# Performance work log

Measured on AMD Instinct MI355X. Metric: run time of the kernel, lower is better.

The kernel has to match this reference:

```python
import jax, jax.numpy as jnp
import numpy as np

M = 41
RHO = M / 2.0          # rho=-1 -> M/2
OVERLAPS = 40

def _get_index():
    S = [(n1, n2)
         for n1 in range(-(M // 2), M // 2)
         for n2 in range(-(M // 2), M // 2)
         if abs(n1 * n2) <= RHO * (M // 2)]
    return np.asarray(S, dtype=np.int32)  # [K,2], K=1600 for defaults

_PAIRS = _get_index()


def setup_inputs() -> dict:
    key = jax.random.key(0)
    ks = jax.random.split(key, 7)
    B, L, N = 2, 2048, 2
    K = _PAIRS.shape[0]
    return {
        "x_real": jax.random.normal(ks[0], (B, L, N), jnp.float32),
        "x_imag": jax.random.normal(ks[1], (B, L, N), jnp.float32),
        "task_info": jax.random.uniform(ks[2], (B, 4), jnp.float32),
        "fc_wr": jax.random.normal(ks[3], (K,), jnp.float32) * 0.02,
        "fc_wi": jax.random.normal(ks[4], (K,), jnp.float32) * 0.02,
        "fc_br": jax.random.normal(ks[5], (1,), jnp.float32) * 0.02,
        "fc_bi": jax.random.normal(ks[6], (1,), jnp.float32) * 0.02,
    }


def reference(x_real, x_imag, task_info, fc_wr, fc_wi, fc_br, fc_bi):
    B, L, N = x_real.shape
    x0 = x_real + 1j * x_imag                      # [B,L,N] complex64
    # get_power: dBm -> Watts per mode
    P = 1e-3 * jnp.power(10.0, task_info[:, 0] / 10.0) / N   # [B]

    xf = jnp.fft.fft(x0, axis=1)                   # [B,L,N]
    idx = jnp.arange(L)
    n1 = jnp.asarray(_PAIRS[:, 0])
    n2 = jnp.asarray(_PAIRS[:, 1])

    # torch.roll(x, s, dim=1)[i] == x[(i - s) % L]; vectorize over all K pairs
    def gather(s):                                  # s: [K]
        return xf[:, (idx[:, None] - s[None, :]) % L, :]   # [B,L,K,N]

    A = gather(n1) * jnp.conj(gather(n1 + n2))      # [B,L,K,N]
    E = (A + jnp.roll(A, 1, axis=-1)) * gather(n2)  # [B,L,K,N]

    w = fc_wr + 1j * fc_wi                          # [K]
    b = fc_br[0] + 1j * fc_bi[0]
    delta = jnp.einsum('blkn,k->bln', E, w) + b     # ComplexLinear K->1
    delta = jnp.fft.ifft(delta, axis=1)

    out = (x0 + delta * P[:, None, None])[:, OVERLAPS // 2 : L - OVERLAPS // 2, :]
    # return real/imag stacked so the baseline output is real-valued
    return jnp.stack([out.real, out.imag], axis=-1)  # [B, L-OVERLAPS, N, 2]
```

## Files before the change

kernel.cpp:

```cpp
#include <hip/hip_runtime.h>


#define L_FFT 2048
#define NB 2
#define NM 2
#define ND 40
#define CROP 20
#define LOUT 2008

__device__ __forceinline__ float2 cmul(float2 a, float2 b) {
    return make_float2(a.x*b.x - a.y*b.y, a.x*b.y + a.y*b.x);
}
__device__ __forceinline__ float2 cmulc(float2 a, float2 b) {
    return make_float2(a.x*b.x + a.y*b.y, a.y*b.x - a.x*b.y);
}

template<int SIGN, int NT>
__device__ void build_tw(float2* tw, int tid) {
    for (int t = tid; t < 1024; t += NT) {
        float ang = (float)(SIGN * t) * 3.0679615757712823e-03f;
        tw[t] = make_float2(__cosf(ang), __sinf(ang));
    }
}

template<int NT>
__device__ float2* fft2048(float2* bufA, float2* bufB, const float2* tw, int tid) {
    float2* src = bufA;
    float2* dst = bufB;
    int m = 1;
    for (int stage = 0; stage < 11; ++stage) {
        __syncthreads();
        #pragma unroll
        for (int it = 0; it < 1024 / NT; ++it) {
            int q = tid + it * NT;
            int k = q & (m - 1);
            int jm = q - k;
            float2 w = tw[jm];
            float2 a = src[q];
            float2 b = src[q + 1024];
            float2 dif = make_float2(a.x - b.x, a.y - b.y);
            dst[2*jm + k]     = make_float2(a.x + b.x, a.y + b.y);
            dst[2*jm + k + m] = make_float2(dif.x*w.x - dif.y*w.y, dif.x*w.y + dif.y*w.x);
        }
        float2* t = src; src = dst; dst = t;
        m <<= 1;
    }
    __syncthreads();
    return src;
}

__global__ __launch_bounds__(1024) void fft_fwd_kernel(const float* __restrict__ xr,
                                                       const float* __restrict__ xi,
                                                       float2* __restrict__ xf,
                                                       float* __restrict__ df) {
    __shared__ float2 bufA[L_FFT];
    __shared__ float2 bufB[L_FFT];
    __shared__ float2 tw[1024];
    int bn = blockIdx.x;
    int b = bn >> 1, n = bn & 1;
    int tid = threadIdx.x;
    #pragma unroll
    for (int i = 0; i < 4; ++i)
        df[bn * (L_FFT * 2) + tid + i * 1024] = 0.f;
    for (int t = tid; t < L_FFT; t += 1024) {
        int gi = (b * L_FFT + t) * NM + n;
        bufA[t] = make_float2(xr[gi], xi[gi]);
    }
    build_tw<-1, 1024>(tw, tid);
    float2* res = fft2048<1024>(bufA, bufB, tw, tid);
    for (int f = tid; f < L_FFT; f += 1024)
        xf[bn * L_FFT + f] = res[f];
}

__global__ __launch_bounds__(256) void gs2_kernel(const float2* __restrict__ xf,
                                                  const float* __restrict__ wr,
                                                  const float* __restrict__ wi,
                                                  float* __restrict__ df) {
    __shared__ float2 xs[2][336];
    __shared__ float2 Gs[296];
    __shared__ float wrs[40], wis[40];
    int blk = blockIdx.x;
    int b   = blk / 320;
    int rem = blk % 320;
    int d   = rem >> 3;
    int l0  = (rem & 7) << 8;
    int dd  = d - 20;
    int tid = threadIdx.x;
    const float2* x0 = xf + (b * 2 + 0) * L_FFT;
    const float2* x1 = xf + (b * 2 + 1) * L_FFT;
    for (int i = tid; i < 336; i += 256) {
        int m = (l0 - 39 + i) & (L_FFT - 1);
        xs[0][i] = x0[m];
        xs[1][i] = x1[m];
    }
    if (tid < 40) { wrs[tid] = wr[tid * 40 + d]; wis[tid] = wi[tid * 40 + d]; }
    __syncthreads();
    for (int j = tid; j < 295; j += 256) {
        float2 g0 = cmulc(xs[0][j + 20], xs[0][j + 20 - dd]);
        float2 g1 = cmulc(xs[1][j + 20], xs[1][j + 20 - dd]);
        Gs[j] = make_float2(g0.x + g1.x, g0.y + g1.y);
    }
    __syncthreads();
    float2 acc = make_float2(0.f, 0.f);
    #pragma unroll
    for (int n1i = 0; n1i < 40; ++n1i) {
        float2 g = Gs[tid + 39 - n1i];
        float wxr = wrs[n1i], wxi = wis[n1i];
        acc.x += wxr * g.x - wxi * g.y;
        acc.y += wxr * g.y + wxi * g.x;
    }
    int xvi = tid + 39 - dd;
    int base = (b * 2) * (L_FFT * 2) + (l0 + tid) * 2;
    float2 xv0 = xs[0][xvi];
    float2 c0 = cmul(acc, xv0);
    unsafeAtomicAdd(&df[base + 0], c0.x);
    unsafeAtomicAdd(&df[base + 1], c0.y);
    float2 xv1 = xs[1][xvi];
    float2 c1 = cmul(acc, xv1);
    unsafeAtomicAdd(&df[base + L_FFT * 2 + 0], c1.x);
    unsafeAtomicAdd(&df[base + L_FFT * 2 + 1], c1.y);
}

__global__ __launch_bounds__(1024) void ifft_out_kernel(const float* __restrict__ df,
                                                        const float* __restrict__ xr,
                                                        const float* __restrict__ xi,
                                                        const float* __restrict__ task,
                                                        float* __restrict__ out) {
    __shared__ float2 bufA[L_FFT];
    __shared__ float2 bufB[L_FFT];
    __shared__ float2 tw[1024];
    int bn = blockIdx.x;
    int b = bn >> 1, n = bn & 1;
    int tid = threadIdx.x;
    const float2* dfreq = (const float2*)df + bn * L_FFT;
    for (int i = tid; i < L_FFT; i += 1024)
        bufA[i] = dfreq[i];
    build_tw<1, 1024>(tw, tid);
    float2* res = fft2048<1024>(bufA, bufB, tw, tid);
    float P = 1e-3f * __powf(10.f, task[b * 4] * 0.1f) * 0.5f;
    float scale = P * (1.0f / (float)L_FFT);
    for (int t = CROP + tid; t < L_FFT - CROP; t += 1024) {
        int gi = (b * L_FFT + t) * NM + n;
        float2 dv = res[t];
        int oi = ((b * LOUT + (t - CROP)) * NM + n) * 2;
        out[oi]     = xr[gi] + dv.x * scale;
        out[oi + 1] = xi[gi] + dv.y * scale;
    }
}

extern "C" void kernel_launch(void* const* d_in, const int* in_sizes, int n_in,
                              void* d_out, int out_size, void* d_ws, size_t ws_size,
                              hipStream_t stream) {
    const float* xr   = (const float*)d_in[0];
    const float* xi   = (const float*)d_in[1];
    const float* task = (const float*)d_in[2];
    const float* wr   = (const float*)d_in[3];
    const float* wi   = (const float*)d_in[4];
    float* out = (float*)d_out;

    float2* ws = (float2*)d_ws;
    float2* xf = ws;
    float*  df = (float*)(ws + 8192);

    hipLaunchKernelGGL(fft_fwd_kernel, dim3(NB * NM), dim3(1024), 0, stream, xr, xi, xf, df);
    hipLaunchKernelGGL(gs2_kernel,     dim3(NB * ND * 8), dim3(256), 0, stream, xf, wr, wi, df);
    hipLaunchKernelGGL(ifft_out_kernel, dim3(NB * NM), dim3(1024), 0, stream, df, xr, xi, task, out);
}
```

Baseline: 22.73 us.

## Fuse FFT, gather-sum and IFFT into one cooperative kernel with grid syncs

```diff
diff --git a/kernel.cpp b/kernel.cpp
--- a/kernel.cpp
+++ b/kernel.cpp
@@ -1,4 +1,7 @@
 #include <hip/hip_runtime.h>
+#include <hip/hip_cooperative_groups.h>
+
+namespace cg = cooperative_groups;
 
 
 #define L_FFT 2048
@@ -7,6 +10,11 @@
 #define ND 40
 #define CROP 20
 #define LOUT 2008
+#define NBLK 160
+#define NT 1024
+#define TILE 1024
+#define SLAB 1103
+#define GSZ 1063
 
 __device__ __forceinline__ float2 cmul(float2 a, float2 b) {
     return make_float2(a.x*b.x - a.y*b.y, a.x*b.y + a.y*b.x);
@@ -15,7 +23,7 @@
     return make_float2(a.x*b.x + a.y*b.y, a.y*b.x - a.x*b.y);
 }
 
-template<int SIGN, int NT>
+template<int SIGN>
 __device__ void build_tw(float2* tw, int tid) {
     for (int t = tid; t < 1024; t += NT) {
         float ang = (float)(SIGN * t) * 3.0679615757712823e-03f;
@@ -23,16 +31,14 @@
     }
 }
 
-template<int NT>
 __device__ float2* fft2048(float2* bufA, float2* bufB, const float2* tw, int tid) {
     float2* src = bufA;
     float2* dst = bufB;
     int m = 1;
     for (int stage = 0; stage < 11; ++stage) {
         __syncthreads();
-        #pragma unroll
-        for (int it = 0; it < 1024 / NT; ++it) {
-            int q = tid + it * NT;
+        {
+            int q = tid;
             int k = q & (m - 1);
             int jm = q - k;
             float2 w = tw[jm];
@@ -49,102 +55,102 @@
     return src;
 }
 
-__global__ __launch_bounds__(1024) void fft_fwd_kernel(const float* __restrict__ xr,
-                                                       const float* __restrict__ xi,
-                                                       float2* __restrict__ xf,
-                                                       float* __restrict__ df) {
-    __shared__ float2 bufA[L_FFT];
-    __shared__ float2 bufB[L_FFT];
-    __shared__ float2 tw[1024];
-    int bn = blockIdx.x;
-    int b = bn >> 1, n = bn & 1;
+__global__ __launch_bounds__(NT) void fused_kernel(const float* __restrict__ xr,
+                                                   const float* __restrict__ xi,
+                                                   const float* __restrict__ task,
+                                                   const float* __restrict__ wr,
+                                                   const float* __restrict__ wi,
+                                                   float* __restrict__ out,
+                                                   float2* __restrict__ xf,
+                                                   float* __restrict__ df) {
+    cg::grid_group grid = cg::this_grid();
+    __shared__ float2 sm[5120];
+    __shared__ float wrs[ND], wis[ND];
+    int blk = blockIdx.x;
     int tid = threadIdx.x;
-    #pragma unroll
-    for (int i = 0; i < 4; ++i)
-        df[bn * (L_FFT * 2) + tid + i * 1024] = 0.f;
-    for (int t = tid; t < L_FFT; t += 1024) {
-        int gi = (b * L_FFT + t) * NM + n;
-        bufA[t] = make_float2(xr[gi], xi[gi]);
+
+    if (blk < NB * NM) {
+        int b = blk >> 1, n = blk & 1;
+        float2* bufA = sm;
+        float2* bufB = sm + 2048;
+        float2* tw   = sm + 4096;
+        float2* dfv = (float2*)df + blk * L_FFT;
+        #pragma unroll
+        for (int i = 0; i < 2; ++i)
+            dfv[tid + i * NT] = make_float2(0.f, 0.f);
+        for (int t = tid; t < L_FFT; t += NT) {
+            int gi = (b * L_FFT + t) * NM + n;
+            bufA[t] = make_float2(xr[gi], xi[gi]);
+        }
+        build_tw<-1>(tw, tid);
+        float2* res = fft2048(bufA, bufB, tw, tid);
+        for (int f = tid; f < L_FFT; f += NT)
+            xf[blk * L_FFT + f] = res[f];
     }
-    build_tw<-1, 1024>(tw, tid);
-    float2* res = fft2048<1024>(bufA, bufB, tw, tid);
-    for (int f = tid; f < L_FFT; f += 1024)
-        xf[bn * L_FFT + f] = res[f];
-}
+    grid.sync();
 
-__global__ __launch_bounds__(256) void gs2_kernel(const float2* __restrict__ xf,
-                                                  const float* __restrict__ wr,
-                                                  const float* __restrict__ wi,
-                                                  float* __restrict__ df) {
-    __shared__ float2 xs[2][336];
-    __shared__ float2 Gs[296];
-    __shared__ float wrs[40], wis[40];
-    int blk = blockIdx.x;
-    int b   = blk / 320;
-    int rem = blk % 320;
-    int d   = rem >> 3;
-    int l0  = (rem & 7) << 8;
-    int dd  = d - 20;
-    int tid = threadIdx.x;
-    const float2* x0 = xf + (b * 2 + 0) * L_FFT;
-    const float2* x1 = xf + (b * 2 + 1) * L_FFT;
-    for (int i = tid; i < 336; i += 256) {
-        int m = (l0 - 39 + i) & (L_FFT - 1);
-        xs[0][i] = x0[m];
-        xs[1][i] = x1[m];
+    {
+        int b   = blk / 80;
+        int rem = blk % 80;
+        int d   = rem >> 1;
+        int l0  = (rem & 1) << 10;
+        int dd  = d - 20;
+        float2* xs0 = sm;
+        float2* xs1 = sm + SLAB;
+        float2* Gs  = sm + 2 * SLAB;
+        const float2* x0 = xf + (b * 2 + 0) * L_FFT;
+        const float2* x1 = xf + (b * 2 + 1) * L_FFT;
+        for (int i = tid; i < SLAB; i += NT) {
+            int m = (l0 - 39 + i) & (L_FFT - 1);
+            xs0[i] = x0[m];
+            xs1[i] = x1[m];
+        }
+        if (tid < ND) { wrs[tid] = wr[tid * ND + d]; wis[tid] = wi[tid * ND + d]; }
+        __syncthreads();
+        for (int j = tid; j < GSZ; j += NT) {
+            float2 g0 = cmulc(xs0[j + 20], xs0[j + 20 - dd]);
+            float2 g1 = cmulc(xs1[j + 20], xs1[j + 20 - dd]);
+            Gs[j] = make_float2(g0.x + g1.x, g0.y + g1.y);
+        }
+        __syncthreads();
+        float2 acc = make_float2(0.f, 0.f);
+        #pragma unroll
+        for (int n1i = 0; n1i < ND; ++n1i) {
+            float2 g = Gs[tid + 39 - n1i];
+            float wxr = wrs[n1i], wxi = wis[n1i];
+            acc.x += wxr * g.x - wxi * g.y;
+            acc.y += wxr * g.y + wxi * g.x;
+        }
+        int xvi  = tid + 39 - dd;
+        int base = (b * 2) * (L_FFT * 2) + (l0 + tid) * 2;
+        float2 c0 = cmul(acc, xs0[xvi]);
+        unsafeAtomicAdd(&df[base + 0], c0.x);
+        unsafeAtomicAdd(&df[base + 1], c0.y);
+        float2 c1 = cmul(acc, xs1[xvi]);
+        unsafeAtomicAdd(&df[base + L_FFT * 2 + 0], c1.x);
+        unsafeAtomicAdd(&df[base + L_FFT * 2 + 1], c1.y);
     }
-    if (tid < 40) { wrs[tid] = wr[tid * 40 + d]; wis[tid] = wi[tid * 40 + d]; }
-    __syncthreads();
-    for (int j = tid; j < 295; j += 256) {
-        float2 g0 = cmulc(xs[0][j + 20], xs[0][j + 20 - dd]);
-        float2 g1 = cmulc(xs[1][j + 20], xs[1][j + 20 - dd]);
-        Gs[j] = make_float2(g0.x + g1.x, g0.y + g1.y);
-    }
-    __syncthreads();
-    float2 acc = make_float2(0.f, 0.f);
-    #pragma unroll
-    for (int n1i = 0; n1i < 40; ++n1i) {
-        float2 g = Gs[tid + 39 - n1i];
-        float wxr = wrs[n1i], wxi = wis[n1i];
-        acc.x += wxr * g.x - wxi * g.y;
-        acc.y += wxr * g.y + wxi * g.x;
-    }
-    int xvi = tid + 39 - dd;
-    int base = (b * 2) * (L_FFT * 2) + (l0 + tid) * 2;
-    float2 xv0 = xs[0][xvi];
-    float2 c0 = cmul(acc, xv0);
-    unsafeAtomicAdd(&df[base + 0], c0.x);
-    unsafeAtomicAdd(&df[base + 1], c0.y);
-    float2 xv1 = xs[1][xvi];
-    float2 c1 = cmul(acc, xv1);
-    unsafeAtomicAdd(&df[base + L_FFT * 2 + 0], c1.x);
-    unsafeAtomicAdd(&df[base + L_FFT * 2 + 1], c1.y);
-}
+    grid.sync();
 
-__global__ __launch_bounds__(1024) void ifft_out_kernel(const float* __restrict__ df,
-                                                        const float* __restrict__ xr,
-                                                        const float* __restrict__ xi,
-                                                        const float* __restrict__ task,
-                                                        float* __restrict__ out) {
-    __shared__ float2 bufA[L_FFT];
-    __shared__ float2 bufB[L_FFT];
-    __shared__ float2 tw[1024];
-    int bn = blockIdx.x;
-    int b = bn >> 1, n = bn & 1;
-    int tid = threadIdx.x;
-    const float2* dfreq = (const float2*)df + bn * L_FFT;
-    for (int i = tid; i < L_FFT; i += 1024)
-        bufA[i] = dfreq[i];
-    build_tw<1, 1024>(tw, tid);
-    float2* res = fft2048<1024>(bufA, bufB, tw, tid);
-    float P = 1e-3f * __powf(10.f, task[b * 4] * 0.1f) * 0.5f;
-    float scale = P * (1.0f / (float)L_FFT);
-    for (int t = CROP + tid; t < L_FFT - CROP; t += 1024) {
-        int gi = (b * L_FFT + t) * NM + n;
-        float2 dv = res[t];
-        int oi = ((b * LOUT + (t - CROP)) * NM + n) * 2;
-        out[oi]     = xr[gi] + dv.x * scale;
-        out[oi + 1] = xi[gi] + dv.y * scale;
+    if (blk < NB * NM) {
+        int b = blk >> 1, n = blk & 1;
+        float2* bufA = sm;
+        float2* bufB = sm + 2048;
+        float2* tw   = sm + 4096;
+        const float2* dfreq = (const float2*)df + blk * L_FFT;
+        for (int i = tid; i < L_FFT; i += NT)
+            bufA[i] = dfreq[i];
+        build_tw<1>(tw, tid);
+        float2* res = fft2048(bufA, bufB, tw, tid);
+        float P = 1e-3f * __powf(10.f, task[b * 4] * 0.1f) * 0.5f;
+        float scale = P * (1.0f / (float)L_FFT);
+        for (int t = CROP + tid; t < L_FFT - CROP; t += NT) {
+            int gi = (b * L_FFT + t) * NM + n;
+            float2 dv = res[t];
+            int oi = ((b * LOUT + (t - CROP)) * NM + n) * 2;
+            out[oi]     = xr[gi] + dv.x * scale;
+            out[oi + 1] = xi[gi] + dv.y * scale;
+        }
     }
 }
 
@@ -162,7 +168,7 @@
     float2* xf = ws;
     float*  df = (float*)(ws + 8192);
 
-    hipLaunchKernelGGL(fft_fwd_kernel, dim3(NB * NM), dim3(1024), 0, stream, xr, xi, xf, df);
-    hipLaunchKernelGGL(gs2_kernel,     dim3(NB * ND * 8), dim3(256), 0, stream, xf, wr, wi, df);
-    hipLaunchKernelGGL(ifft_out_kernel, dim3(NB * NM), dim3(1024), 0, stream, df, xr, xi, task, out);
+    void* args[] = { (void*)&xr, (void*)&xi, (void*)&task, (void*)&wr, (void*)&wi,
+                     (void*)&out, (void*)&xf, (void*)&df };
+    hipLaunchCooperativeKernel((void*)fused_kernel, dim3(NBLK), dim3(NT), args, 0, stream);
 }
```

Measured after the change: 61.82 us. +171.9%, slower.

## Switch FFTs to radix-4 Stockham and merge four shift offsets per gs2 block

Applied to the files above, without the earlier changes.

```diff
diff --git a/kernel.cpp b/kernel.cpp
--- a/kernel.cpp
+++ b/kernel.cpp
@@ -15,131 +15,165 @@
     return make_float2(a.x*b.x + a.y*b.y, a.y*b.x - a.x*b.y);
 }
 
-template<int SIGN, int NT>
+template<int SIGN>
 __device__ void build_tw(float2* tw, int tid) {
-    for (int t = tid; t < 1024; t += NT) {
-        float ang = (float)(SIGN * t) * 3.0679615757712823e-03f;
-        tw[t] = make_float2(__cosf(ang), __sinf(ang));
-    }
-}
-
-template<int NT>
-__device__ float2* fft2048(float2* bufA, float2* bufB, const float2* tw, int tid) {
+    if (tid < 512) {
+        float ang = (float)(SIGN * tid) * 3.0679615757712823e-03f;
+        tw[tid] = make_float2(__cosf(ang), __sinf(ang));
+    }
+}
+
+template<int SIGN>
+__device__ float2* fft2048_r4(float2* bufA, float2* bufB, const float2* tw, int tid) {
     float2* src = bufA;
     float2* dst = bufB;
-    int m = 1;
-    for (int stage = 0; stage < 11; ++stage) {
+    #pragma unroll
+    for (int m = 1; m <= 256; m *= 4) {
         __syncthreads();
-        #pragma unroll
-        for (int it = 0; it < 1024 / NT; ++it) {
-            int q = tid + it * NT;
-            int k = q & (m - 1);
-            int jm = q - k;
-            float2 w = tw[jm];
-            float2 a = src[q];
-            float2 b = src[q + 1024];
-            float2 dif = make_float2(a.x - b.x, a.y - b.y);
-            dst[2*jm + k]     = make_float2(a.x + b.x, a.y + b.y);
-            dst[2*jm + k + m] = make_float2(dif.x*w.x - dif.y*w.y, dif.x*w.y + dif.y*w.x);
-        }
+        int k2 = tid & (m - 1);
+        int jm = tid - k2;
+        float2 A = src[tid];
+        float2 C = src[tid + 512];
+        float2 B = src[tid + 1024];
+        float2 D = src[tid + 1536];
+        float2 T0 = make_float2(A.x + B.x, A.y + B.y);
+        float2 T1 = make_float2(A.x - B.x, A.y - B.y);
+        float2 T2 = make_float2(C.x + D.x, C.y + D.y);
+        float2 cd = make_float2(C.x - D.x, C.y - D.y);
+        float2 T3 = (SIGN < 0) ? make_float2(cd.y, -cd.x)
+                               : make_float2(-cd.y, cd.x);
+        float2 w1 = tw[jm];
+        float2 w2 = cmul(w1, w1);
+        float2 w3 = cmul(w2, w1);
+        int base = 4 * jm + k2;
+        dst[base]         = make_float2(T0.x + T2.x, T0.y + T2.y);
+        dst[base + m]     = cmul(make_float2(T1.x + T3.x, T1.y + T3.y), w1);
+        dst[base + 2*m]   = cmul(make_float2(T0.x - T2.x, T0.y - T2.y), w2);
+        dst[base + 3*m]   = cmul(make_float2(T1.x - T3.x, T1.y - T3.y), w3);
         float2* t = src; src = dst; dst = t;
-        m <<= 1;
     }
     __syncthreads();
-    return src;
-}
-
-__global__ __launch_bounds__(1024) void fft_fwd_kernel(const float* __restrict__ xr,
-                                                       const float* __restrict__ xi,
-                                                       float2* __restrict__ xf,
-                                                       float* __restrict__ df) {
+    #pragma unroll
+    for (int it = 0; it < 2; ++it) {
+        int q = tid + it * 512;
+        float2 a = src[q];
+        float2 b = src[q + 1024];
+        dst[q]        = make_float2(a.x + b.x, a.y + b.y);
+        dst[q + 1024] = make_float2(a.x - b.x, a.y - b.y);
+    }
+    float2* res = dst;
+    __syncthreads();
+    return res;
+}
+
+__global__ __launch_bounds__(512) void fft_fwd_kernel(const float* __restrict__ xr,
+                                                      const float* __restrict__ xi,
+                                                      float2* __restrict__ xf,
+                                                      float* __restrict__ df) {
     __shared__ float2 bufA[L_FFT];
     __shared__ float2 bufB[L_FFT];
-    __shared__ float2 tw[1024];
+    __shared__ float2 tw[512];
     int bn = blockIdx.x;
     int b = bn >> 1, n = bn & 1;
     int tid = threadIdx.x;
     #pragma unroll
-    for (int i = 0; i < 4; ++i)
-        df[bn * (L_FFT * 2) + tid + i * 1024] = 0.f;
-    for (int t = tid; t < L_FFT; t += 1024) {
+    for (int i = 0; i < 8; ++i)
+        df[bn * (L_FFT * 2) + tid + i * 512] = 0.f;
+    #pragma unroll
+    for (int it = 0; it < 4; ++it) {
+        int t = tid + it * 512;
         int gi = (b * L_FFT + t) * NM + n;
         bufA[t] = make_float2(xr[gi], xi[gi]);
     }
-    build_tw<-1, 1024>(tw, tid);
-    float2* res = fft2048<1024>(bufA, bufB, tw, tid);
-    for (int f = tid; f < L_FFT; f += 1024)
+    build_tw<-1>(tw, tid);
+    float2* res = fft2048_r4<-1>(bufA, bufB, tw, tid);
+    #pragma unroll
+    for (int it = 0; it < 4; ++it) {
+        int f = tid + it * 512;
         xf[bn * L_FFT + f] = res[f];
+    }
 }
 
 __global__ __launch_bounds__(256) void gs2_kernel(const float2* __restrict__ xf,
                                                   const float* __restrict__ wr,
                                                   const float* __restrict__ wi,
                                                   float* __restrict__ df) {
-    __shared__ float2 xs[2][336];
+    __shared__ float2 xs0[336], xs1[336];
     __shared__ float2 Gs[296];
-    __shared__ float wrs[40], wis[40];
+    __shared__ float wrs[40][4], wis[40][4];
     int blk = blockIdx.x;
-    int b   = blk / 320;
-    int rem = blk % 320;
-    int d   = rem >> 3;
+    int b   = blk / 80;
+    int rem = blk % 80;
+    int dq  = rem >> 3;
     int l0  = (rem & 7) << 8;
-    int dd  = d - 20;
     int tid = threadIdx.x;
     const float2* x0 = xf + (b * 2 + 0) * L_FFT;
     const float2* x1 = xf + (b * 2 + 1) * L_FFT;
     for (int i = tid; i < 336; i += 256) {
         int m = (l0 - 39 + i) & (L_FFT - 1);
-        xs[0][i] = x0[m];
-        xs[1][i] = x1[m];
-    }
-    if (tid < 40) { wrs[tid] = wr[tid * 40 + d]; wis[tid] = wi[tid * 40 + d]; }
+        xs0[i] = x0[m];
+        xs1[i] = x1[m];
+    }
+    if (tid < 160) {
+        int n1i = tid >> 2, di = tid & 3;
+        wrs[n1i][di] = wr[n1i * ND + dq * 4 + di];
+        wis[n1i][di] = wi[n1i * ND + dq * 4 + di];
+    }
     __syncthreads();
-    for (int j = tid; j < 295; j += 256) {
-        float2 g0 = cmulc(xs[0][j + 20], xs[0][j + 20 - dd]);
-        float2 g1 = cmulc(xs[1][j + 20], xs[1][j + 20 - dd]);
-        Gs[j] = make_float2(g0.x + g1.x, g0.y + g1.y);
-    }
-    __syncthreads();
-    float2 acc = make_float2(0.f, 0.f);
-    #pragma unroll
-    for (int n1i = 0; n1i < 40; ++n1i) {
-        float2 g = Gs[tid + 39 - n1i];
-        float wxr = wrs[n1i], wxi = wis[n1i];
-        acc.x += wxr * g.x - wxi * g.y;
-        acc.y += wxr * g.y + wxi * g.x;
-    }
-    int xvi = tid + 39 - dd;
+    float2 a0 = make_float2(0.f, 0.f);
+    float2 a1 = make_float2(0.f, 0.f);
+    #pragma unroll
+    for (int di = 0; di < 4; ++di) {
+        int d  = dq * 4 + di;
+        int dd = d - 20;
+        for (int j = tid; j < 295; j += 256) {
+            float2 g0 = cmulc(xs0[j + 20], xs0[j + 20 - dd]);
+            float2 g1 = cmulc(xs1[j + 20], xs1[j + 20 - dd]);
+            Gs[j] = make_float2(g0.x + g1.x, g0.y + g1.y);
+        }
+        __syncthreads();
+        float2 acc = make_float2(0.f, 0.f);
+        #pragma unroll
+        for (int n1i = 0; n1i < ND; ++n1i) {
+            float2 g = Gs[tid + 39 - n1i];
+            float wxr = wrs[n1i][di], wxi = wis[n1i][di];
+            acc.x += wxr * g.x - wxi * g.y;
+            acc.y += wxr * g.y + wxi * g.x;
+        }
+        int xvi = tid + 39 - dd;
+        float2 c0 = cmul(acc, xs0[xvi]);
+        float2 c1 = cmul(acc, xs1[xvi]);
+        a0.x += c0.x; a0.y += c0.y;
+        a1.x += c1.x; a1.y += c1.y;
+        __syncthreads();
+    }
     int base = (b * 2) * (L_FFT * 2) + (l0 + tid) * 2;
-    float2 xv0 = xs[0][xvi];
-    float2 c0 = cmul(acc, xv0);
-    unsafeAtomicAdd(&df[base + 0], c0.x);
-    unsafeAtomicAdd(&df[base + 1], c0.y);
-    float2 xv1 = xs[1][xvi];
-    float2 c1 = cmul(acc, xv1);
-    unsafeAtomicAdd(&df[base + L_FFT * 2 + 0], c1.x);
-    unsafeAtomicAdd(&df[base + L_FFT * 2 + 1], c1.y);
-}
-
-__global__ __launch_bounds__(1024) void ifft_out_kernel(const float* __restrict__ df,
-                                                        const float* __restrict__ xr,
-                                                        const float* __restrict__ xi,
-                                                        const float* __restrict__ task,
-                                                        float* __restrict__ out) {
+    unsafeAtomicAdd(&df[base + 0], a0.x);
+    unsafeAtomicAdd(&df[base + 1], a0.y);
+    unsafeAtomicAdd(&df[base + L_FFT * 2 + 0], a1.x);
+    unsafeAtomicAdd(&df[base + L_FFT * 2 + 1], a1.y);
+}
+
+__global__ __launch_bounds__(512) void ifft_out_kernel(const float* __restrict__ df,
+                                                       const float* __restrict__ xr,
+                                                       const float* __restrict__ xi,
+                                                       const float* __restrict__ task,
+                                                       float* __restrict__ out) {
     __shared__ float2 bufA[L_FFT];
     __shared__ float2 bufB[L_FFT];
-    __shared__ float2 tw[1024];
+    __shared__ float2 tw[512];
     int bn = blockIdx.x;
     int b = bn >> 1, n = bn & 1;
     int tid = threadIdx.x;
     const float2* dfreq = (const float2*)df + bn * L_FFT;
-    for (int i = tid; i < L_FFT; i += 1024)
-        bufA[i] = dfreq[i];
-    build_tw<1, 1024>(tw, tid);
-    float2* res = fft2048<1024>(bufA, bufB, tw, tid);
+    #pragma unroll
+    for (int it = 0; it < 4; ++it)
+        bufA[tid + it * 512] = dfreq[tid + it * 512];
+    build_tw<1>(tw, tid);
+    float2* res = fft2048_r4<1>(bufA, bufB, tw, tid);
     float P = 1e-3f * __powf(10.f, task[b * 4] * 0.1f) * 0.5f;
     float scale = P * (1.0f / (float)L_FFT);
-    for (int t = CROP + tid; t < L_FFT - CROP; t += 1024) {
+    for (int t = CROP + tid; t < L_FFT - CROP; t += 512) {
         int gi = (b * L_FFT + t) * NM + n;
         float2 dv = res[t];
         int oi = ((b * LOUT + (t - CROP)) * NM + n) * 2;
@@ -162,7 +196,7 @@
     float2* xf = ws;
     float*  df = (float*)(ws + 8192);
 
-    hipLaunchKernelGGL(fft_fwd_kernel, dim3(NB * NM), dim3(1024), 0, stream, xr, xi, xf, df);
-    hipLaunchKernelGGL(gs2_kernel,     dim3(NB * ND * 8), dim3(256), 0, stream, xf, wr, wi, df);
-    hipLaunchKernelGGL(ifft_out_kernel, dim3(NB * NM), dim3(1024), 0, stream, df, xr, xi, task, out);
-}
+    hipLaunchKernelGGL(fft_fwd_kernel,  dim3(NB * NM), dim3(512), 0, stream, xr, xi, xf, df);
+    hipLaunchKernelGGL(gs2_kernel,      dim3(160), dim3(256), 0, stream, xf, wr, wi, df);
+    hipLaunchKernelGGL(ifft_out_kernel, dim3(NB * NM), dim3(512), 0, stream, df, xr, xi, task, out);
+}
```

Measured after the change: 23.01 us. About the same (+1.2%).
